# Optimization experiments

Hardware: AMD Instinct MI355X
Metric: run time of the kernel (lower is better)

The kernel has to match this reference:

```python
import jax, jax.numpy as jnp
import numpy as np

N = 131072      # octree nodes at this depth
C_IN = 256      # in_channels == out_channels
C_B = 64        # bottleneck channels = out_channels // 4
K = 27          # 3x3x3 octree kernel neighborhood
EPS = 1e-5


def _bn(x, g, b, m, v):
    # inference-style BatchNorm with given running stats
    return (x - m) * (g * jax.lax.rsqrt(v + EPS)) + b


def setup_inputs() -> dict:
    key = jax.random.key(0)
    ks = jax.random.split(key, 20)
    inp = {
        "data": jax.random.normal(ks[0], (N, C_IN), dtype=jnp.float32),
        "neigh": jax.random.randint(ks[1], (N, K), 0, N, dtype=jnp.int32),
        "depth": 6,
        # conv1x1a (Linear, no bias) + BN
        "w1": jax.random.normal(ks[2], (C_IN, C_B), dtype=jnp.float32) * 0.05,
        "bn1_g": jax.random.uniform(ks[3], (C_B,), dtype=jnp.float32) + 0.5,
        "bn1_b": jax.random.normal(ks[4], (C_B,), dtype=jnp.float32) * 0.1,
        "bn1_m": jax.random.normal(ks[5], (C_B,), dtype=jnp.float32) * 0.1,
        "bn1_v": jax.random.uniform(ks[6], (C_B,), dtype=jnp.float32) + 0.5,
        # octree conv3x3 (27-neighbor gather + GEMM, no bias) + BN
        "w3": jax.random.normal(ks[7], (K, C_B, C_B), dtype=jnp.float32) * 0.02,
        "bn2_g": jax.random.uniform(ks[8], (C_B,), dtype=jnp.float32) + 0.5,
        "bn2_b": jax.random.normal(ks[9], (C_B,), dtype=jnp.float32) * 0.1,
        "bn2_m": jax.random.normal(ks[10], (C_B,), dtype=jnp.float32) * 0.1,
        "bn2_v": jax.random.uniform(ks[11], (C_B,), dtype=jnp.float32) + 0.5,
        # conv1x1b + BN (no ReLU)
        "w2": jax.random.normal(ks[12], (C_B, C_IN), dtype=jnp.float32) * 0.05,
        "bn3_g": jax.random.uniform(ks[13], (C_IN,), dtype=jnp.float32) + 0.5,
        "bn3_b": jax.random.normal(ks[14], (C_IN,), dtype=jnp.float32) * 0.1,
        "bn3_m": jax.random.normal(ks[15], (C_IN,), dtype=jnp.float32) * 0.1,
        "bn3_v": jax.random.uniform(ks[16], (C_IN,), dtype=jnp.float32) + 0.5,
    }
    return inp


def reference(data, neigh, depth, w1, bn1_g, bn1_b, bn1_m, bn1_v,
              w3, bn2_g, bn2_b, bn2_m, bn2_v,
              w2, bn3_g, bn3_b, bn3_m, bn3_v):
    # conv1x1a + BN + ReLU
    c1 = jax.nn.relu(_bn(data @ w1, bn1_g, bn1_b, bn1_m, bn1_v))  # [N, C_B]
    # octree conv3x3: gather 27 neighbors then contract with [K, C_B, C_B]
    gathered = c1[neigh]                                          # [N, K, C_B]
    c2 = jnp.einsum('nkc,kcd->nd', gathered, w3)                  # [N, C_B]
    c2 = jax.nn.relu(_bn(c2, bn2_g, bn2_b, bn2_m, bn2_v))
    # conv1x1b + BN (no relu)
    c3 = _bn(c2 @ w2, bn3_g, bn3_b, bn3_m, bn3_v)                 # [N, C_IN]
    # residual (in_channels == out_channels -> identity shortcut) + ReLU
    return jax.nn.relu(c3 + data)
```

## Files before the change

kernel.cpp:

```cpp
#include <hip/hip_runtime.h>

#define CIN 256
#define CB 64
#define KNB 27

typedef __attribute__((ext_vector_type(8))) short short8_t;
typedef __attribute__((ext_vector_type(4))) float f32x4;
typedef __attribute__((ext_vector_type(4))) int   i32x4;

__device__ inline unsigned short f2bf(float f) {
    union { float f; unsigned u; } x; x.f = f;
    unsigned r = x.u + 0x7fffu + ((x.u >> 16) & 1u);
    return (unsigned short)(r >> 16);
}
__device__ inline float bf2f(unsigned short h) {
    union { unsigned u; float f; } x; x.u = ((unsigned)h) << 16; return x.f;
}
__device__ inline f32x4 mfma16(short8_t a, short8_t b, f32x4 c) {
    return __builtin_amdgcn_mfma_f32_16x16x32_bf16(a, b, c, 0, 0, 0);
}
__device__ inline i32x4 mfma_i8(i32x4 a, i32x4 b, i32x4 c) {
    return __builtin_amdgcn_mfma_i32_16x16x64_i8(a, b, c, 0, 0, 0);
}

__global__ __launch_bounds__(256) void prep_a_kernel(
    const float* __restrict__ w1, const float* __restrict__ w2,
    const float* __restrict__ g1, const float* __restrict__ b1, const float* __restrict__ m1, const float* __restrict__ v1,
    const float* __restrict__ g2, const float* __restrict__ b2, const float* __restrict__ m2, const float* __restrict__ v2,
    const float* __restrict__ g3, const float* __restrict__ b3, const float* __restrict__ m3, const float* __restrict__ v3,
    unsigned short* __restrict__ w1p, unsigned short* __restrict__ w2p,
    float* __restrict__ bias1, float* __restrict__ bias2, float* __restrict__ bias3)
{
    int t = blockIdx.x * 256 + threadIdx.x;
    if (t < 16384) {
        int j = t & 7, lane = (t >> 3) & 63, tt = (t >> 9) & 3, s = t >> 11;
        int c = s * 32 + (lane >> 4) * 8 + j;
        int d = tt * 16 + (lane & 15);
        float sc = g1[d] * rsqrtf(v1[d] + 1e-5f);
        w1p[t] = f2bf(w1[c * CB + d] * sc);
    } else if (t < 32768) {
        int u = t - 16384;
        int j = u & 7, lane = (u >> 3) & 63, mt = (u >> 9) & 15, s = u >> 13;
        int c = s * 32 + (lane >> 4) * 8 + j;
        int d = mt * 16 + (lane & 15);
        float sc = g3[d] * rsqrtf(v3[d] + 1e-5f);
        w2p[u] = f2bf(w2[c * CIN + d] * sc);
    } else if (t < 33152) {
        int u = t - 32768;
        if (u < 64)       { float sc = g1[u] * rsqrtf(v1[u] + 1e-5f); bias1[u] = b1[u] - m1[u] * sc; }
        else if (u < 128) { int d = u - 64;  float sc = g2[d] * rsqrtf(v2[d] + 1e-5f); bias2[d] = b2[d] - m2[d] * sc; }
        else              { int d = u - 128; float sc = g3[d] * rsqrtf(v3[d] + 1e-5f); bias3[d] = b3[d] - m3[d] * sc; }
    }
}

__global__ __launch_bounds__(256) void prep_bq_kernel(
    const float* __restrict__ w3, const float* __restrict__ g2, const float* __restrict__ v2,
    signed char* __restrict__ w3q, unsigned* __restrict__ amax)
{
    __shared__ float sc2[64];
    __shared__ float sm[4];
    int tid = threadIdx.x;
    if (tid < 64) sc2[tid] = g2[tid] * rsqrtf(v2[tid] + 1e-5f);
    __syncthreads();

    const float4* w34 = (const float4*)w3;
    float m = 0.f;
    for (int e = tid; e < KNB * CB * CB / 4; e += 256) {
        float4 v = w34[e];
        int d0 = (e * 4) & 63;
        m = fmaxf(m, fabsf(v.x * sc2[d0]));
        m = fmaxf(m, fabsf(v.y * sc2[d0 + 1]));
        m = fmaxf(m, fabsf(v.z * sc2[d0 + 2]));
        m = fmaxf(m, fabsf(v.w * sc2[d0 + 3]));
    }
#pragma unroll
    for (int off = 32; off; off >>= 1) m = fmaxf(m, __shfl_xor(m, off));
    if ((tid & 63) == 0) sm[tid >> 6] = m;
    __syncthreads();
    float mm = fmaxf(fmaxf(sm[0], sm[1]), fmaxf(sm[2], sm[3]));
    float inv = mm > 0.f ? 127.f / mm : 0.f;

    int u = blockIdx.x * 256 + tid;
    int j = u & 15, lane = (u >> 4) & 63, tile = (u >> 10) & 3, k = u >> 12;
    int c = (lane >> 4) * 16 + j;
    int d = tile * 16 + (lane & 15);
    int q = __float2int_rn(w3[(k * CB + c) * CB + d] * sc2[d] * inv);
    q = q > 127 ? 127 : (q < -127 ? -127 : q);
    w3q[u] = (signed char)q;
    if (blockIdx.x == 0 && tid == 0) amax[1] = __float_as_uint(mm);
}

__global__ __launch_bounds__(256) void k1_conv1x1a(
    const float* __restrict__ data, const unsigned short* __restrict__ w1p,
    const float* __restrict__ bias1, unsigned short* __restrict__ c1b,
    float* __restrict__ blockmax)
{
    __shared__ short8_t w1s[2048];
    __shared__ float smax[4];
    int tid = threadIdx.x;
    const short8_t* wsrc = (const short8_t*)w1p;
#pragma unroll
    for (int i = 0; i < 8; i++) w1s[tid + i * 256] = wsrc[tid + i * 256];

    int lane = tid & 63, wave = tid >> 6;
    int g = lane >> 4, r = lane & 15;
    int rowbase = blockIdx.x * 128 + wave * 32;
    f32x4 acc[2][4] = {};
    __syncthreads();

#pragma unroll
    for (int s = 0; s < 8; s++) {
        short8_t a[2];
#pragma unroll
        for (int sub = 0; sub < 2; sub++) {
            const float* ap = data + (size_t)(rowbase + sub * 16 + r) * CIN + s * 32 + g * 8;
            float4 f0 = *(const float4*)ap;
            float4 f1 = *(const float4*)(ap + 4);
            short8_t av;
            av[0] = (short)f2bf(f0.x); av[1] = (short)f2bf(f0.y);
            av[2] = (short)f2bf(f0.z); av[3] = (short)f2bf(f0.w);
            av[4] = (short)f2bf(f1.x); av[5] = (short)f2bf(f1.y);
            av[6] = (short)f2bf(f1.z); av[7] = (short)f2bf(f1.w);
            a[sub] = av;
        }
#pragma unroll
        for (int t = 0; t < 4; t++) {
            short8_t b = w1s[(s * 4 + t) * 64 + lane];
            acc[0][t] = mfma16(a[0], b, acc[0][t]);
            acc[1][t] = mfma16(a[1], b, acc[1][t]);
        }
    }

    float mloc = 0.f;
#pragma unroll
    for (int sub = 0; sub < 2; sub++)
#pragma unroll
        for (int t = 0; t < 4; t++) {
            int col = t * 16 + r;
            float bs = bias1[col];
#pragma unroll
            for (int i = 0; i < 4; i++) {
                int row = rowbase + sub * 16 + g * 4 + i;
                float v = fmaxf(acc[sub][t][i] + bs, 0.f);
                mloc = fmaxf(mloc, v);
                c1b[row * CB + col] = f2bf(v);
            }
        }
#pragma unroll
    for (int off = 32; off; off >>= 1) mloc = fmaxf(mloc, __shfl_xor(mloc, off));
    if (lane == 0) smax[wave] = mloc;
    __syncthreads();
    if (tid == 0)
        blockmax[blockIdx.x] = fmaxf(fmaxf(smax[0], smax[1]), fmaxf(smax[2], smax[3]));
}

__global__ __launch_bounds__(256) void quant_c1_kernel(
    const unsigned short* __restrict__ c1b, const float* __restrict__ blockmax,
    signed char* __restrict__ c1q, unsigned* __restrict__ amax)
{
    __shared__ float sm[4];
    int tid = threadIdx.x;
    float4 bm = ((const float4*)blockmax)[tid];
    float m = fmaxf(fmaxf(bm.x, bm.y), fmaxf(bm.z, bm.w));
#pragma unroll
    for (int off = 32; off; off >>= 1) m = fmaxf(m, __shfl_xor(m, off));
    if ((tid & 63) == 0) sm[tid >> 6] = m;
    __syncthreads();
    float s1 = fmaxf(fmaxf(sm[0], sm[1]), fmaxf(sm[2], sm[3]));
    float inv = s1 > 0.f ? 127.f / s1 : 0.f;

    int t = blockIdx.x * 256 + tid;
    const short8_t* src = (const short8_t*)c1b;
    short8_t v0 = src[t * 2], v1 = src[t * 2 + 1];
    int ow[4];
#pragma unroll
    for (int h = 0; h < 4; h++) {
        int w = 0;
#pragma unroll
        for (int e = 0; e < 4; e++) {
            unsigned short hv = (unsigned short)((h < 2 ? v0 : v1)[(h & 1) * 4 + e]);
            int q = __float2int_rn(bf2f(hv) * inv);
            q = q > 127 ? 127 : q;
            w |= (q & 0xff) << (e * 8);
        }
        ow[h] = w;
    }
    ((int4*)c1q)[t] = make_int4(ow[0], ow[1], ow[2], ow[3]);
    if (blockIdx.x == 0 && tid == 0) amax[0] = __float_as_uint(s1);
}

__global__ __launch_bounds__(64, 4) void k2_conv3x3(
    const signed char* __restrict__ c1q, const int* __restrict__ neigh,
    const signed char* __restrict__ w3q, const float* __restrict__ bias2,
    const unsigned* __restrict__ amax, unsigned short* __restrict__ c2b)
{
    __shared__ int nidx[32 * KNB];
    int tid = threadIdx.x;
    int rowbase = blockIdx.x * 32;

    const int4* nsrc = (const int4*)(neigh + (size_t)rowbase * KNB);
#pragma unroll
    for (int i = 0; i < 4; i++) {
        int p = tid + i * 64;
        if (p < 216) ((int4*)nidx)[p] = nsrc[p];
    }

    int lane = tid;
    int g = lane >> 4, r = lane & 15;
    float sf = __uint_as_float(amax[0]) * __uint_as_float(amax[1]) * (1.f / (127.f * 127.f));
    __syncthreads();

    const i32x4* bq = (const i32x4*)w3q;
    i32x4 iacc[2][4] = {};

#pragma unroll
    for (int k = 0; k < KNB; k++) {
        i32x4 b0 = bq[k * 256 + lane];
        i32x4 b1 = bq[k * 256 + 64 + lane];
        i32x4 b2 = bq[k * 256 + 128 + lane];
        i32x4 b3 = bq[k * 256 + 192 + lane];
        int i0 = nidx[r * KNB + k];
        int i1 = nidx[(16 + r) * KNB + k];
        i32x4 a0 = *(const i32x4*)(c1q + (size_t)i0 * CB + g * 16);
        i32x4 a1 = *(const i32x4*)(c1q + (size_t)i1 * CB + g * 16);
        iacc[0][0] = mfma_i8(a0, b0, iacc[0][0]);
        iacc[1][0] = mfma_i8(a1, b0, iacc[1][0]);
        iacc[0][1] = mfma_i8(a0, b1, iacc[0][1]);
        iacc[1][1] = mfma_i8(a1, b1, iacc[1][1]);
        iacc[0][2] = mfma_i8(a0, b2, iacc[0][2]);
        iacc[1][2] = mfma_i8(a1, b2, iacc[1][2]);
        iacc[0][3] = mfma_i8(a0, b3, iacc[0][3]);
        iacc[1][3] = mfma_i8(a1, b3, iacc[1][3]);
    }

#pragma unroll
    for (int sub = 0; sub < 2; sub++)
#pragma unroll
        for (int t = 0; t < 4; t++) {
            int col = t * 16 + r;
            float bs = bias2[col];
#pragma unroll
            for (int i = 0; i < 4; i++) {
                int row = rowbase + sub * 16 + g * 4 + i;
                float v = fmaxf((float)iacc[sub][t][i] * sf + bs, 0.f);
                c2b[row * CB + col] = f2bf(v);
            }
        }
}

__global__ __launch_bounds__(256) void k3_conv1x1b(
    const unsigned short* __restrict__ c2b, const unsigned short* __restrict__ w2p,
    const float* __restrict__ bias3, const float* __restrict__ data,
    float* __restrict__ out)
{
    __shared__ float otile[64 * 260];
    int tid = threadIdx.x;
    int lane = tid & 63, wave = tid >> 6;
    int g = lane >> 4, r = lane & 15;
    int rowbase = blockIdx.x * 64;

    const short8_t* abase = (const short8_t*)w2p;
    short8_t bfr[4][2];
#pragma unroll
    for (int sub = 0; sub < 4; sub++)
#pragma unroll
        for (int s = 0; s < 2; s++)
            bfr[sub][s] = *(const short8_t*)(c2b + (size_t)(rowbase + sub * 16 + r) * CB + s * 32 + g * 8);

    f32x4 acc2[4][4] = {};
#pragma unroll
    for (int s = 0; s < 2; s++)
#pragma unroll
        for (int mt = 0; mt < 4; mt++) {
            short8_t a = abase[(s * 16 + wave * 4 + mt) * 64 + lane];
#pragma unroll
            for (int sub = 0; sub < 4; sub++)
                acc2[sub][mt] = mfma16(a, bfr[sub][s], acc2[sub][mt]);
        }

#pragma unroll
    for (int sub = 0; sub < 4; sub++)
#pragma unroll
        for (int mt = 0; mt < 4; mt++) {
            int col0 = (wave * 4 + mt) * 16 + g * 4;
            int lrow = sub * 16 + r;
            float4 bs = *(const float4*)(bias3 + col0);
            f32x4 v = acc2[sub][mt];
            float4 sv;
            sv.x = v[0] + bs.x; sv.y = v[1] + bs.y;
            sv.z = v[2] + bs.z; sv.w = v[3] + bs.w;
            *(float4*)&otile[lrow * 260 + col0] = sv;
        }
    __syncthreads();

    const float4* dsrc = (const float4*)(data + (size_t)rowbase * CIN);
    float4* dst = (float4*)(out + (size_t)rowbase * CIN);
#pragma unroll
    for (int p = 0; p < 16; p++) {
        int idx = p * 256 + tid;
        int row = idx >> 6, c4 = (idx & 63) << 2;
        float4 ov = *(const float4*)&otile[row * 260 + c4];
        float4 dv = dsrc[idx];
        float4 res;
        res.x = fmaxf(ov.x + dv.x, 0.f);
        res.y = fmaxf(ov.y + dv.y, 0.f);
        res.z = fmaxf(ov.z + dv.z, 0.f);
        res.w = fmaxf(ov.w + dv.w, 0.f);
        dst[idx] = res;
    }
}

extern "C" void kernel_launch(void* const* d_in, const int* in_sizes, int n_in,
                              void* d_out, int out_size, void* d_ws, size_t ws_size,
                              hipStream_t stream)
{
    const float* data = (const float*)d_in[0];
    const int* neigh  = (const int*)d_in[1];
    const float* w1 = (const float*)d_in[3];
    const float* g1 = (const float*)d_in[4];
    const float* b1 = (const float*)d_in[5];
    const float* m1 = (const float*)d_in[6];
    const float* v1 = (const float*)d_in[7];
    const float* w3 = (const float*)d_in[8];
    const float* g2 = (const float*)d_in[9];
    const float* b2 = (const float*)d_in[10];
    const float* m2 = (const float*)d_in[11];
    const float* v2 = (const float*)d_in[12];
    const float* w2 = (const float*)d_in[13];
    const float* g3 = (const float*)d_in[14];
    const float* b3 = (const float*)d_in[15];
    const float* m3 = (const float*)d_in[16];
    const float* v3 = (const float*)d_in[17];
    float* out = (float*)d_out;

    char* ws = (char*)d_ws;
    unsigned short* c1b = (unsigned short*)ws;
    unsigned short* c2b = (unsigned short*)ws;
    signed char*    c1q = (signed char*)(ws + 16777216);
    unsigned short* w1p = (unsigned short*)(ws + 25165824);
    signed char*    w3q = (signed char*)(ws + 25198592);
    unsigned short* w2p = (unsigned short*)(ws + 25309184);
    float* bias1 = (float*)(ws + 25341952);
    float* bias2 = bias1 + 64;
    float* bias3 = bias1 + 128;
    unsigned* amax = (unsigned*)(ws + 25343488);
    float* blockmax = (float*)(ws + 25343552);

    int n = in_sizes[0] / CIN;

    hipLaunchKernelGGL(prep_a_kernel, dim3(130), dim3(256), 0, stream,
                       w1, w2, g1, b1, m1, v1, g2, b2, m2, v2, g3, b3, m3, v3,
                       w1p, w2p, bias1, bias2, bias3);
    hipLaunchKernelGGL(prep_bq_kernel, dim3(432), dim3(256), 0, stream,
                       w3, g2, v2, w3q, amax);
    hipLaunchKernelGGL(k1_conv1x1a, dim3(n / 128), dim3(256), 0, stream,
                       data, w1p, bias1, c1b, blockmax);
    hipLaunchKernelGGL(quant_c1_kernel, dim3(2048), dim3(256), 0, stream,
                       c1b, blockmax, c1q, amax);
    hipLaunchKernelGGL(k2_conv3x3, dim3(n / 32), dim3(64), 0, stream,
                       c1q, neigh, w3q, bias2, amax, c2b);
    hipLaunchKernelGGL(k3_conv1x1b, dim3(n / 64), dim3(256), 0, stream,
                       c2b, w2p, bias3, data, out);
}
```

Measured before the change: 175.6 us.

## Split octree conv gather into two index-range passes with 64-row tiles

```diff
diff --git a/kernel.cpp b/kernel.cpp
--- a/kernel.cpp
+++ b/kernel.cpp
@@ -189,60 +189,67 @@
     if (blockIdx.x == 0 && tid == 0) amax[0] = __float_as_uint(s1);
 }
 
-__global__ __launch_bounds__(64, 4) void k2_conv3x3(
+__global__ __launch_bounds__(64) void k2_conv3x3(
     const signed char* __restrict__ c1q, const int* __restrict__ neigh,
     const signed char* __restrict__ w3q, const float* __restrict__ bias2,
     const unsigned* __restrict__ amax, unsigned short* __restrict__ c2b)
 {
-    __shared__ int nidx[32 * KNB];
-    int tid = threadIdx.x;
-    int rowbase = blockIdx.x * 32;
+    __shared__ int nidx[64 * KNB];
+    int tid = threadIdx.x;
+    int rowbase = blockIdx.x * 64;
 
     const int4* nsrc = (const int4*)(neigh + (size_t)rowbase * KNB);
 #pragma unroll
-    for (int i = 0; i < 4; i++) {
+    for (int i = 0; i < 7; i++) {
         int p = tid + i * 64;
-        if (p < 216) ((int4*)nidx)[p] = nsrc[p];
-    }
-
-    int lane = tid;
-    int g = lane >> 4, r = lane & 15;
+        if (p < 432) ((int4*)nidx)[p] = nsrc[p];
+    }
+
+    int g = tid >> 4, r = tid & 15;
     float sf = __uint_as_float(amax[0]) * __uint_as_float(amax[1]) * (1.f / (127.f * 127.f));
     __syncthreads();
 
     const i32x4* bq = (const i32x4*)w3q;
-    i32x4 iacc[2][4] = {};
-
-#pragma unroll
-    for (int k = 0; k < KNB; k++) {
-        i32x4 b0 = bq[k * 256 + lane];
-        i32x4 b1 = bq[k * 256 + 64 + lane];
-        i32x4 b2 = bq[k * 256 + 128 + lane];
-        i32x4 b3 = bq[k * 256 + 192 + lane];
-        int i0 = nidx[r * KNB + k];
-        int i1 = nidx[(16 + r) * KNB + k];
-        i32x4 a0 = *(const i32x4*)(c1q + (size_t)i0 * CB + g * 16);
-        i32x4 a1 = *(const i32x4*)(c1q + (size_t)i1 * CB + g * 16);
-        iacc[0][0] = mfma_i8(a0, b0, iacc[0][0]);
-        iacc[1][0] = mfma_i8(a1, b0, iacc[1][0]);
-        iacc[0][1] = mfma_i8(a0, b1, iacc[0][1]);
-        iacc[1][1] = mfma_i8(a1, b1, iacc[1][1]);
-        iacc[0][2] = mfma_i8(a0, b2, iacc[0][2]);
-        iacc[1][2] = mfma_i8(a1, b2, iacc[1][2]);
-        iacc[0][3] = mfma_i8(a0, b3, iacc[0][3]);
-        iacc[1][3] = mfma_i8(a1, b3, iacc[1][3]);
-    }
-
-#pragma unroll
-    for (int sub = 0; sub < 2; sub++)
+    i32x4 iacc[4][4] = {};
+
+    for (int pass = 0; pass < 2; pass++) {
+        int lo = pass << 16;
+        int hi = lo + 65536;
+#pragma unroll
+        for (int k = 0; k < KNB; k++) {
+            i32x4 b0 = bq[k * 256 + tid];
+            i32x4 b1 = bq[k * 256 + 64 + tid];
+            i32x4 b2 = bq[k * 256 + 128 + tid];
+            i32x4 b3 = bq[k * 256 + 192 + tid];
+            i32x4 a[4];
+#pragma unroll
+            for (int rg = 0; rg < 4; rg++) {
+                int idx = nidx[(rg * 16 + r) * KNB + k];
+                i32x4 av = {0, 0, 0, 0};
+                if (idx >= lo && idx < hi)
+                    av = *(const i32x4*)(c1q + (size_t)idx * CB + g * 16);
+                a[rg] = av;
+            }
+#pragma unroll
+            for (int rg = 0; rg < 4; rg++) {
+                iacc[rg][0] = mfma_i8(a[rg], b0, iacc[rg][0]);
+                iacc[rg][1] = mfma_i8(a[rg], b1, iacc[rg][1]);
+                iacc[rg][2] = mfma_i8(a[rg], b2, iacc[rg][2]);
+                iacc[rg][3] = mfma_i8(a[rg], b3, iacc[rg][3]);
+            }
+        }
+    }
+
+#pragma unroll
+    for (int rg = 0; rg < 4; rg++)
 #pragma unroll
         for (int t = 0; t < 4; t++) {
             int col = t * 16 + r;
             float bs = bias2[col];
 #pragma unroll
             for (int i = 0; i < 4; i++) {
-                int row = rowbase + sub * 16 + g * 4 + i;
-                float v = fmaxf((float)iacc[sub][t][i] * sf + bs, 0.f);
+                int row = rowbase + rg * 16 + g * 4 + i;
+                float v = fmaxf((float)iacc[rg][t][i] * sf + bs, 0.f);
                 c2b[row * CB + col] = f2bf(v);
             }
         }
@@ -357,7 +364,7 @@
                        data, w1p, bias1, c1b, blockmax);
     hipLaunchKernelGGL(quant_c1_kernel, dim3(2048), dim3(256), 0, stream,
                        c1b, blockmax, c1q, amax);
-    hipLaunchKernelGGL(k2_conv3x3, dim3(n / 32), dim3(64), 0, stream,
+    hipLaunchKernelGGL(k2_conv3x3, dim3(n / 64), dim3(64), 0, stream,
                        c1q, neigh, w3q, bias2, amax, c2b);
     hipLaunchKernelGGL(k3_conv1x1b, dim3(n / 64), dim3(256), 0, stream,
                        c2b, w2p, bias3, data, out);
```

After: 403.6 us. +129.9%, slower.
